# Optimization experiments

Hardware: AMD Instinct MI355X
Metric: run time of the kernel (lower is better)

Reference implementation:

```python
import jax, jax.numpy as jnp
import numpy as np

N_NODES = 100000
N_EDGES = 1600000
NFEAT, NHID, NCLASS, NL = 128, 64, 40, 6


def setup_inputs() -> dict:
    key = jax.random.key(0)
    ks = jax.random.split(key, 12)
    x = jax.random.normal(ks[0], (N_NODES, NFEAT), dtype=jnp.float32)
    edge_row = jax.random.randint(ks[1], (N_EDGES,), 0, N_NODES)
    edge_col = jax.random.randint(ks[2], (N_EDGES,), 0, N_NODES)
    # positive values mimicking a degree-normalized adjacency
    edge_val = jax.random.uniform(ks[3], (N_EDGES,), dtype=jnp.float32) / 16.0
    s1 = 1.0 / np.sqrt(NFEAT)
    sh = 1.0 / np.sqrt(NHID)
    W1 = jax.random.uniform(ks[4], (NFEAT, NHID), minval=-s1, maxval=s1, dtype=jnp.float32)
    b1 = jax.random.uniform(ks[5], (NHID,), minval=-s1, maxval=s1, dtype=jnp.float32)
    Wm = jax.random.uniform(ks[6], (NL, NHID, NHID), minval=-sh, maxval=sh, dtype=jnp.float32)
    bm = jax.random.uniform(ks[7], (NL, NHID), minval=-sh, maxval=sh, dtype=jnp.float32)
    W2 = jax.random.uniform(ks[8], (NHID, NCLASS), minval=-sh, maxval=sh, dtype=jnp.float32)
    b2 = jax.random.uniform(ks[9], (NCLASS,), minval=-sh, maxval=sh, dtype=jnp.float32)
    return {"x": x, "edge_row": edge_row, "edge_col": edge_col, "edge_val": edge_val,
            "W1": W1, "b1": b1, "Wm": Wm, "bm": bm, "W2": W2, "b2": b2}


def _gconv(h, row, col, val, W, b):
    # GraphConvolution: support = h @ W ; out = spmm(adj, support) + b
    support = h @ W                       # [N, out]
    msgs = val[:, None] * support[col]    # [E, out] gather
    agg = jax.ops.segment_sum(msgs, row, num_segments=h.shape[0])  # scatter-add
    return agg + b


def reference(x, edge_row, edge_col, edge_val, W1, b1, Wm, bm, W2, b2):
    # gc1: relu (dropout is identity in eval mode)
    h1 = jax.nn.relu(_gconv(x, edge_row, edge_col, edge_val, W1, b1))
    # first middle layer (module index 2): relu, no residual
    h2 = jax.nn.relu(_gconv(h1, edge_row, edge_col, edge_val, Wm[0], bm[0]))
    prev2, prev = h1, h2
    # remaining middle layers: relu + residual to two layers back
    for k in range(1, NL):
        h = jax.nn.relu(_gconv(prev, edge_row, edge_col, edge_val, Wm[k], bm[k])) + prev2
        prev2, prev = prev, h
    out = _gconv(prev, edge_row, edge_col, edge_val, W2, b2)  # gc2, no relu
    return jax.nn.log_softmax(out, axis=1)
```

## Files before the change

kernel.cpp:

```cpp
#include <hip/hip_runtime.h>
#include <hip/hip_bf16.h>
#include <math.h>

#define N_NODES 100000
#define N_EDGES 1600000
#define NFEAT 128
#define NHID  64
#define NCLASS 40
#define NL 6

#define NBUK 256
#define RPB  391
#define EPP  (N_EDGES / NBUK)
#define EP_PAD 256
#define NTILES (N_NODES / 16)

typedef __attribute__((ext_vector_type(8))) short short8;
typedef __attribute__((ext_vector_type(8))) unsigned short ushort8v;
typedef __attribute__((ext_vector_type(4))) float floatx4;

__device__ __forceinline__ float bfbits(unsigned short u) {
  return __uint_as_float((unsigned int)u << 16);
}
__device__ __forceinline__ short f2bs(float f) {
  __hip_bfloat16 h = __float2bfloat16(f);
  return *reinterpret_cast<short*>(&h);
}

__global__ __launch_bounds__(1024) void p0_hist_k(const int* __restrict__ row,
                                                  int* __restrict__ h2d) {
  __shared__ int h[NBUK];
  const int i = blockIdx.x, t = threadIdx.x;
  if (t < NBUK) h[t] = 0;
  __syncthreads();
  const int e0 = i * EPP, e1 = e0 + EPP;
  for (int e = e0 + t; e < e1; e += 1024) atomicAdd(&h[row[e] / RPB], 1);
  __syncthreads();
  if (t < NBUK) h2d[i * NBUK + t] = h[t];
}

__global__ __launch_bounds__(256) void k1_scanb_k(int* __restrict__ h2d,
                                                  int* __restrict__ btot) {
  __shared__ int sd[256];
  const int b = blockIdx.x, t = threadIdx.x;
  int v = h2d[t * NBUK + b];
  sd[t] = v;
  __syncthreads();
  for (int off = 1; off < 256; off <<= 1) {
    int a = (t >= off) ? sd[t - off] : 0;
    __syncthreads();
    sd[t] += a;
    __syncthreads();
  }
  h2d[t * NBUK + b] = sd[t] - v;
  if (t == 255) btot[b] = sd[255];
}

__global__ __launch_bounds__(256) void k2_scanbase_k(const int* __restrict__ btot,
                                                     int* __restrict__ bbase,
                                                     int2* __restrict__ ep) {
  __shared__ int sd[256];
  const int t = threadIdx.x;
  int v = btot[t];
  sd[t] = v;
  __syncthreads();
  for (int off = 1; off < 256; off <<= 1) {
    int a = (t >= off) ? sd[t - off] : 0;
    __syncthreads();
    sd[t] += a;
    __syncthreads();
  }
  bbase[t] = sd[t] - v;
  if (t == 255) bbase[256] = sd[255];
  if (t < EP_PAD) ep[N_EDGES + t] = make_int2(0, 0);
}

__global__ __launch_bounds__(1024) void p2_part_k(
    const int* __restrict__ row, const int* __restrict__ col,
    const float* __restrict__ val, const int* __restrict__ h2d,
    const int* __restrict__ bbase, int2* __restrict__ pcv,
    unsigned short* __restrict__ plr) {
  __shared__ int cur[NBUK];
  const int i = blockIdx.x, t = threadIdx.x;
  if (t < NBUK) cur[t] = bbase[t] + h2d[i * NBUK + t];
  __syncthreads();
  const int e0 = i * EPP, e1 = e0 + EPP;
  for (int e = e0 + t; e < e1; e += 1024) {
    int r = row[e];
    int b = r / RPB;
    int p = atomicAdd(&cur[b], 1);
    pcv[p] = make_int2(col[e], __float_as_int(val[e]));
    plr[p] = (unsigned short)(r - b * RPB);
  }
}

__global__ __launch_bounds__(1024) void p3_fine_k(const int2* __restrict__ pcv,
                                                  const unsigned short* __restrict__ plr,
                                                  const int* __restrict__ bbase,
                                                  int* __restrict__ rp,
                                                  int2* __restrict__ ep) {
  __shared__ int cnt[RPB];
  __shared__ int cur[RPB];
  const int b = blockIdx.x, t = threadIdx.x;
  const int ebeg = bbase[b], eend = bbase[b + 1];
  const int r0 = b * RPB;
  const int nloc = min(RPB, N_NODES - r0);

  for (int i = t; i < RPB; i += 1024) cnt[i] = 0;
  __syncthreads();
  for (int j = ebeg + t; j < eend; j += 1024) atomicAdd(&cnt[plr[j]], 1);
  __syncthreads();

  if (t < 64) {
    const int base_ = t * 7;
    int v[7], s = 0;
#pragma unroll
    for (int k = 0; k < 7; ++k) {
      int idx = base_ + k;
      v[k] = (idx < RPB) ? cnt[idx] : 0;
      s += v[k];
    }
    int incl = s;
#pragma unroll
    for (int off = 1; off < 64; off <<= 1) {
      int y = __shfl_up(incl, off);
      if (t >= off) incl += y;
    }
    int run = incl - s;
#pragma unroll
    for (int k = 0; k < 7; ++k) {
      int idx = base_ + k;
      if (idx < RPB) cnt[idx] = run;
      run += v[k];
    }
  }
  __syncthreads();

  for (int i = t; i < nloc; i += 1024) {
    rp[r0 + i] = ebeg + cnt[i];
    cur[i] = cnt[i];
  }
  if (b == 0 && t == 0) rp[N_NODES] = N_EDGES;
  __syncthreads();

  for (int j = ebeg + t; j < eend; j += 1024) {
    int lr = plr[j];
    int p = atomicAdd(&cur[lr], 1);
    ep[ebeg + p] = pcv[j];
  }
}

__global__ __launch_bounds__(256) void gemm_l1(const float* __restrict__ X,
                                               const float* __restrict__ W,
                                               unsigned short* __restrict__ S) {
  const int lane = threadIdx.x & 63;
  const int quad = lane >> 4;
  const int m = lane & 15;

  short8 bf[4][4];
#pragma unroll
  for (int t = 0; t < 4; ++t)
#pragma unroll
    for (int h = 0; h < 4; ++h)
#pragma unroll
      for (int j = 0; j < 8; ++j)
        bf[t][h][j] = f2bs(W[(h * 32 + quad * 8 + j) * 64 + t * 16 + m]);

  const int wid = blockIdx.x * 4 + (threadIdx.x >> 6);
  for (int tile = wid; tile < NTILES; tile += gridDim.x * 4) {
    const int r0 = tile * 16;
    const float* xr = X + (size_t)(r0 + m) * 128;
    short8 af[4];
#pragma unroll
    for (int h = 0; h < 4; ++h) {
      const float* p = xr + h * 32 + quad * 8;
      float4 a = *(const float4*)p;
      float4 b = *(const float4*)(p + 4);
      af[h][0] = f2bs(a.x); af[h][1] = f2bs(a.y);
      af[h][2] = f2bs(a.z); af[h][3] = f2bs(a.w);
      af[h][4] = f2bs(b.x); af[h][5] = f2bs(b.y);
      af[h][6] = f2bs(b.z); af[h][7] = f2bs(b.w);
    }
#pragma unroll
    for (int t = 0; t < 4; ++t) {
      floatx4 acc = {0.0f, 0.0f, 0.0f, 0.0f};
#pragma unroll
      for (int h = 0; h < 4; ++h)
        acc = __builtin_amdgcn_mfma_f32_16x16x32_bf16(af[h], bf[t][h], acc, 0, 0, 0);
#pragma unroll
      for (int r = 0; r < 4; ++r)
        S[(size_t)(r0 + quad * 4 + r) * 64 + t * 16 + m] = (unsigned short)f2bs(acc[r]);
    }
  }
}

template <int COLS>
__global__ __launch_bounds__(256) void gemm_bf(const unsigned short* __restrict__ Hb,
                                               const float* __restrict__ W,
                                               unsigned short* __restrict__ S) {
  const int lane = threadIdx.x & 63;
  const int quad = lane >> 4;
  const int m = lane & 15;

  short8 bf[4][2];
#pragma unroll
  for (int t = 0; t < 4; ++t) {
    const int cc = t * 16 + m;
#pragma unroll
    for (int h = 0; h < 2; ++h)
#pragma unroll
      for (int j = 0; j < 8; ++j)
        bf[t][h][j] = (COLS == 64 || cc < COLS)
                          ? f2bs(W[(h * 32 + quad * 8 + j) * COLS + cc])
                          : (short)0;
  }

  const int wid = blockIdx.x * 4 + (threadIdx.x >> 6);
  for (int tile = wid; tile < NTILES; tile += gridDim.x * 4) {
    const int r0 = tile * 16;
    const unsigned short* hr = Hb + (size_t)(r0 + m) * 64 + quad * 8;
    short8 af0 = *(const short8*)hr;
    short8 af1 = *(const short8*)(hr + 32);
#pragma unroll
    for (int t = 0; t < 4; ++t) {
      floatx4 acc = {0.0f, 0.0f, 0.0f, 0.0f};
      acc = __builtin_amdgcn_mfma_f32_16x16x32_bf16(af0, bf[t][0], acc, 0, 0, 0);
      acc = __builtin_amdgcn_mfma_f32_16x16x32_bf16(af1, bf[t][1], acc, 0, 0, 0);
#pragma unroll
      for (int r = 0; r < 4; ++r)
        S[(size_t)(r0 + quad * 4 + r) * 64 + t * 16 + m] = (unsigned short)f2bs(acc[r]);
    }
  }
}

template <bool RES>
__global__ __launch_bounds__(256) void spmm8_k(
    const unsigned short* __restrict__ S, const int2* __restrict__ ep,
    const int* __restrict__ rp, const float* __restrict__ bias,
    unsigned short* __restrict__ Hbout) {
  const int lane = threadIdx.x & 63;
  const int og = lane >> 3;
  const int i8 = lane & 7;
  const int sg = og & 3;
  const bool isB = og >= 4;
  const int pair = blockIdx.x * 4 + (threadIdx.x >> 6);
  const int nodeA = pair * 2;
  const int sA = rp[nodeA], sB = rp[nodeA + 1], eB = rp[nodeA + 2];
  const int myNode = nodeA + (isB ? 1 : 0);
  const int myBeg = isB ? sB : sA;
  const int myEnd = isB ? eB : sB;
  const int iters = (max(sB - sA, eB - sB) + 7) >> 3;

  float a[8] = {0, 0, 0, 0, 0, 0, 0, 0};
  int e = myBeg + sg;
  int ec = e;
  int2 q0 = ep[e], q1 = ep[e + 4];
  int2 n0 = ep[e + 8], n1 = ep[e + 12];
  ushort8v s0 = *(const ushort8v*)(S + ((size_t)q0.x * 64 + i8 * 8));
  ushort8v s1 = *(const ushort8v*)(S + ((size_t)q1.x * 64 + i8 * 8));
  e += 8;

  for (int it = 0; it < iters; ++it) {
    int2 m0 = ep[e + 8], m1 = ep[e + 12];
    ushort8v t0 = *(const ushort8v*)(S + ((size_t)n0.x * 64 + i8 * 8));
    ushort8v t1 = *(const ushort8v*)(S + ((size_t)n1.x * 64 + i8 * 8));
    float v0 = (ec < myEnd) ? __int_as_float(q0.y) : 0.0f;
    float v1 = (ec + 4 < myEnd) ? __int_as_float(q1.y) : 0.0f;
#pragma unroll
    for (int j = 0; j < 8; ++j) a[j] = fmaf(v0, bfbits(s0[j]), a[j]);
#pragma unroll
    for (int j = 0; j < 8; ++j) a[j] = fmaf(v1, bfbits(s1[j]), a[j]);
    q0 = n0; q1 = n1; n0 = m0; n1 = m1; s0 = t0; s1 = t1;
    ec += 8; e += 8;
  }

#pragma unroll
  for (int j = 0; j < 8; ++j) {
    a[j] += __shfl_xor(a[j], 8);
    a[j] += __shfl_xor(a[j], 16);
  }

  if (sg == 0) {
    float4 b0 = ((const float4*)bias)[i8 * 2];
    float4 b1 = ((const float4*)bias)[i8 * 2 + 1];
    float h[8];
    h[0] = fmaxf(a[0] + b0.x, 0.0f); h[1] = fmaxf(a[1] + b0.y, 0.0f);
    h[2] = fmaxf(a[2] + b0.z, 0.0f); h[3] = fmaxf(a[3] + b0.w, 0.0f);
    h[4] = fmaxf(a[4] + b1.x, 0.0f); h[5] = fmaxf(a[5] + b1.y, 0.0f);
    h[6] = fmaxf(a[6] + b1.z, 0.0f); h[7] = fmaxf(a[7] + b1.w, 0.0f);
    if (RES) {
      ushort8v r = ((const ushort8v*)Hbout)[(size_t)myNode * 8 + i8];
#pragma unroll
      for (int j = 0; j < 8; ++j) h[j] += bfbits(r[j]);
    }
    ushort8v hb;
#pragma unroll
    for (int j = 0; j < 8; ++j) hb[j] = (unsigned short)f2bs(h[j]);
    ((ushort8v*)Hbout)[(size_t)myNode * 8 + i8] = hb;
  }
}

__global__ __launch_bounds__(256) void spmm_final_k(
    const unsigned short* __restrict__ S, const int2* __restrict__ ep,
    const int* __restrict__ rp, const float* __restrict__ b2,
    float* __restrict__ out) {
  const int lane = threadIdx.x & 63;
  const int og = lane >> 3;
  const int i8 = lane & 7;
  const int sg = og & 3;
  const bool isB = og >= 4;
  const int pair = blockIdx.x * 4 + (threadIdx.x >> 6);
  const int nodeA = pair * 2;
  const int sA = rp[nodeA], sB = rp[nodeA + 1], eB = rp[nodeA + 2];
  const int myNode = nodeA + (isB ? 1 : 0);
  const int myBeg = isB ? sB : sA;
  const int myEnd = isB ? eB : sB;
  const int iters = (max(sB - sA, eB - sB) + 7) >> 3;

  float a[8] = {0, 0, 0, 0, 0, 0, 0, 0};
  int e = myBeg + sg;
  int ec = e;
  int2 q0 = ep[e], q1 = ep[e + 4];
  int2 n0 = ep[e + 8], n1 = ep[e + 12];
  ushort8v s0 = *(const ushort8v*)(S + ((size_t)q0.x * 64 + i8 * 8));
  ushort8v s1 = *(const ushort8v*)(S + ((size_t)q1.x * 64 + i8 * 8));
  e += 8;

  for (int it = 0; it < iters; ++it) {
    int2 m0 = ep[e + 8], m1 = ep[e + 12];
    ushort8v t0 = *(const ushort8v*)(S + ((size_t)n0.x * 64 + i8 * 8));
    ushort8v t1 = *(const ushort8v*)(S + ((size_t)n1.x * 64 + i8 * 8));
    float v0 = (ec < myEnd) ? __int_as_float(q0.y) : 0.0f;
    float v1 = (ec + 4 < myEnd) ? __int_as_float(q1.y) : 0.0f;
#pragma unroll
    for (int j = 0; j < 8; ++j) a[j] = fmaf(v0, bfbits(s0[j]), a[j]);
#pragma unroll
    for (int j = 0; j < 8; ++j) a[j] = fmaf(v1, bfbits(s1[j]), a[j]);
    q0 = n0; q1 = n1; n0 = m0; n1 = m1; s0 = t0; s1 = t1;
    ec += 8; e += 8;
  }

#pragma unroll
  for (int j = 0; j < 8; ++j) {
    a[j] += __shfl_xor(a[j], 8);
    a[j] += __shfl_xor(a[j], 16);
  }

  const bool valid = (i8 < 5);
  float l[8];
  float mx = -INFINITY;
  if (valid) {
    float4 c0 = ((const float4*)b2)[i8 * 2];
    float4 c1 = ((const float4*)b2)[i8 * 2 + 1];
    l[0] = a[0] + c0.x; l[1] = a[1] + c0.y; l[2] = a[2] + c0.z; l[3] = a[3] + c0.w;
    l[4] = a[4] + c1.x; l[5] = a[5] + c1.y; l[6] = a[6] + c1.z; l[7] = a[7] + c1.w;
#pragma unroll
    for (int j = 0; j < 8; ++j) mx = fmaxf(mx, l[j]);
  }
#pragma unroll
  for (int off = 1; off < 8; off <<= 1) mx = fmaxf(mx, __shfl_xor(mx, off));
  float sum = 0.0f;
  if (valid) {
#pragma unroll
    for (int j = 0; j < 8; ++j) sum += expf(l[j] - mx);
  }
#pragma unroll
  for (int off = 1; off < 8; off <<= 1) sum += __shfl_xor(sum, off);

  if (sg == 0 && valid) {
    float lg = mx + logf(sum);
    ((float4*)out)[(size_t)myNode * 10 + i8 * 2] =
        make_float4(l[0] - lg, l[1] - lg, l[2] - lg, l[3] - lg);
    ((float4*)out)[(size_t)myNode * 10 + i8 * 2 + 1] =
        make_float4(l[4] - lg, l[5] - lg, l[6] - lg, l[7] - lg);
  }
}

extern "C" void kernel_launch(void* const* d_in, const int* in_sizes, int n_in,
                              void* d_out, int out_size, void* d_ws, size_t ws_size,
                              hipStream_t stream) {
  const float* x    = (const float*)d_in[0];
  const int*   erow = (const int*)d_in[1];
  const int*   ecol = (const int*)d_in[2];
  const float* eval = (const float*)d_in[3];
  const float* W1   = (const float*)d_in[4];
  const float* b1   = (const float*)d_in[5];
  const float* Wm   = (const float*)d_in[6];
  const float* bm   = (const float*)d_in[7];
  const float* W2   = (const float*)d_in[8];
  const float* b2   = (const float*)d_in[9];
  float* out = (float*)d_out;

  char* ws = (char*)d_ws;
  size_t off = 0;
  auto alloc = [&](size_t bytes) {
    void* p = ws + off;
    off = (off + bytes + 255) & ~(size_t)255;
    return p;
  };
  int*  rp    = (int*)alloc((N_NODES + 1) * sizeof(int));
  int*  h2d   = (int*)alloc((size_t)NBUK * NBUK * sizeof(int));
  int*  btot  = (int*)alloc(NBUK * sizeof(int));
  int*  bbase = (int*)alloc((NBUK + 1) * sizeof(int));
  int2* ep    = (int2*)alloc((size_t)(N_EDGES + EP_PAD) * sizeof(int2));
  char* U     = (char*)alloc((size_t)N_EDGES * sizeof(int2) +
                             (((size_t)N_EDGES * sizeof(unsigned short) + 255) & ~(size_t)255));
  int2* pcv = (int2*)U;
  unsigned short* plr = (unsigned short*)(U + (size_t)N_EDGES * sizeof(int2));
  unsigned short* S = (unsigned short*)U;
  unsigned short* B0 = (unsigned short*)alloc((size_t)N_NODES * 64 * sizeof(unsigned short));
  unsigned short* B1 = (unsigned short*)alloc((size_t)N_NODES * 64 * sizeof(unsigned short));

  const int SPMM_GRID = N_NODES / 8;
  const int GEMM_GRID = 512;

  p0_hist_k<<<NBUK, 1024, 0, stream>>>(erow, h2d);
  k1_scanb_k<<<NBUK, 256, 0, stream>>>(h2d, btot);
  k2_scanbase_k<<<1, 256, 0, stream>>>(btot, bbase, ep);
  p2_part_k<<<NBUK, 1024, 0, stream>>>(erow, ecol, eval, h2d, bbase, pcv, plr);
  p3_fine_k<<<NBUK, 1024, 0, stream>>>(pcv, plr, bbase, rp, ep);

  gemm_l1<<<GEMM_GRID, 256, 0, stream>>>(x, W1, S);
  spmm8_k<false><<<SPMM_GRID, 256, 0, stream>>>(S, ep, rp, b1, B0);

  gemm_bf<64><<<GEMM_GRID, 256, 0, stream>>>(B0, Wm, S);
  spmm8_k<false><<<SPMM_GRID, 256, 0, stream>>>(S, ep, rp, bm, B1);

  gemm_bf<64><<<GEMM_GRID, 256, 0, stream>>>(B1, Wm + 1 * 4096, S);
  spmm8_k<true><<<SPMM_GRID, 256, 0, stream>>>(S, ep, rp, bm + 1 * 64, B0);

  gemm_bf<64><<<GEMM_GRID, 256, 0, stream>>>(B0, Wm + 2 * 4096, S);
  spmm8_k<true><<<SPMM_GRID, 256, 0, stream>>>(S, ep, rp, bm + 2 * 64, B1);

  gemm_bf<64><<<GEMM_GRID, 256, 0, stream>>>(B1, Wm + 3 * 4096, S);
  spmm8_k<true><<<SPMM_GRID, 256, 0, stream>>>(S, ep, rp, bm + 3 * 64, B0);

  gemm_bf<64><<<GEMM_GRID, 256, 0, stream>>>(B0, Wm + 4 * 4096, S);
  spmm8_k<true><<<SPMM_GRID, 256, 0, stream>>>(S, ep, rp, bm + 4 * 64, B1);

  gemm_bf<64><<<GEMM_GRID, 256, 0, stream>>>(B1, Wm + 5 * 4096, S);
  spmm8_k<true><<<SPMM_GRID, 256, 0, stream>>>(S, ep, rp, bm + 5 * 64, B0);

  gemm_bf<40><<<GEMM_GRID, 256, 0, stream>>>(B0, W2, S);
  spmm_final_k<<<SPMM_GRID, 256, 0, stream>>>(S, ep, rp, b2, out);
}
```

Baseline: 492.1 us.

## Pair nodes by degree via counting sort to balance SpMM wavefront work

Adds a degree counting sort (histogram, scan, scatter) that builds a node order in descending degree, so each wavefront processes two nodes of similar degree. The SpMM kernels read node pairs from this order, which reduces idle half-wave iterations caused by mismatched degrees. Heavy nodes are also scheduled first. The cost is three extra small kernels and an indirection. Output rows are now written in scattered order, and neighboring wavefronts no longer touch contiguous rows.

```diff
diff --git a/kernel.cpp b/kernel.cpp
--- a/kernel.cpp
+++ b/kernel.cpp
@@ -14,6 +14,7 @@
 #define EPP  (N_EDGES / NBUK)
 #define EP_PAD 256
 #define NTILES (N_NODES / 16)
+#define DBINS 256
 
 typedef __attribute__((ext_vector_type(8))) short short8;
 typedef __attribute__((ext_vector_type(8))) unsigned short ushort8v;
@@ -58,9 +59,11 @@
 
 __global__ __launch_bounds__(256) void k2_scanbase_k(const int* __restrict__ btot,
                                                      int* __restrict__ bbase,
-                                                     int2* __restrict__ ep) {
+                                                     int2* __restrict__ ep,
+                                                     int* __restrict__ dh) {
   __shared__ int sd[256];
   const int t = threadIdx.x;
+  dh[t] = 0;
   int v = btot[t];
   sd[t] = v;
   __syncthreads();
@@ -150,6 +153,49 @@
   }
 }
 
+__global__ __launch_bounds__(256) void deg_hist_k(const int* __restrict__ rp,
+                                                  int* __restrict__ dh) {
+  __shared__ int h[DBINS];
+  const int t = threadIdx.x;
+  h[t] = 0;
+  __syncthreads();
+  const int i = blockIdx.x * 256 + t;
+  if (i < N_NODES) {
+    int d = rp[i + 1] - rp[i];
+    int bin = (DBINS - 1) - min(d, DBINS - 1);
+    atomicAdd(&h[bin], 1);
+  }
+  __syncthreads();
+  if (h[t]) atomicAdd(&dh[t], h[t]);
+}
+
+__global__ __launch_bounds__(256) void deg_scan_k(int* __restrict__ dh) {
+  __shared__ int sd[256];
+  const int t = threadIdx.x;
+  int v = dh[t];
+  sd[t] = v;
+  __syncthreads();
+  for (int off = 1; off < 256; off <<= 1) {
+    int a = (t >= off) ? sd[t - off] : 0;
+    __syncthreads();
+    sd[t] += a;
+    __syncthreads();
+  }
+  dh[t] = sd[t] - v;
+}
+
+__global__ __launch_bounds__(256) void deg_scatter_k(const int* __restrict__ rp,
+                                                     int* __restrict__ dh,
+                                                     int* __restrict__ order) {
+  const int i = blockIdx.x * 256 + threadIdx.x;
+  if (i < N_NODES) {
+    int d = rp[i + 1] - rp[i];
+    int bin = (DBINS - 1) - min(d, DBINS - 1);
+    int p = atomicAdd(&dh[bin], 1);
+    order[p] = i;
+  }
+}
+
 __global__ __launch_bounds__(256) void gemm_l1(const float* __restrict__ X,
                                                const float* __restrict__ W,
                                                unsigned short* __restrict__ S) {
@@ -236,7 +282,8 @@
 template <bool RES>
 __global__ __launch_bounds__(256) void spmm8_k(
     const unsigned short* __restrict__ S, const int2* __restrict__ ep,
-    const int* __restrict__ rp, const float* __restrict__ bias,
+    const int* __restrict__ rp, const int* __restrict__ order,
+    const float* __restrict__ bias,
     unsigned short* __restrict__ Hbout) {
   const int lane = threadIdx.x & 63;
   const int og = lane >> 3;
@@ -244,12 +291,13 @@
   const int sg = og & 3;
   const bool isB = og >= 4;
   const int pair = blockIdx.x * 4 + (threadIdx.x >> 6);
-  const int nodeA = pair * 2;
-  const int sA = rp[nodeA], sB = rp[nodeA + 1], eB = rp[nodeA + 2];
-  const int myNode = nodeA + (isB ? 1 : 0);
+  const int2 ab = ((const int2*)order)[pair];
+  const int sA = rp[ab.x], eA = rp[ab.x + 1];
+  const int sB = rp[ab.y], eB = rp[ab.y + 1];
+  const int myNode = isB ? ab.y : ab.x;
   const int myBeg = isB ? sB : sA;
-  const int myEnd = isB ? eB : sB;
-  const int iters = (max(sB - sA, eB - sB) + 7) >> 3;
+  const int myEnd = isB ? eB : eA;
+  const int iters = (max(eA - sA, eB - sB) + 7) >> 3;
 
   float a[8] = {0, 0, 0, 0, 0, 0, 0, 0};
   int e = myBeg + sg;
@@ -302,20 +350,21 @@
 
 __global__ __launch_bounds__(256) void spmm_final_k(
     const unsigned short* __restrict__ S, const int2* __restrict__ ep,
-    const int* __restrict__ rp, const float* __restrict__ b2,
-    float* __restrict__ out) {
+    const int* __restrict__ rp, const int* __restrict__ order,
+    const float* __restrict__ b2, float* __restrict__ out) {
   const int lane = threadIdx.x & 63;
   const int og = lane >> 3;
   const int i8 = lane & 7;
   const int sg = og & 3;
   const bool isB = og >= 4;
   const int pair = blockIdx.x * 4 + (threadIdx.x >> 6);
-  const int nodeA = pair * 2;
-  const int sA = rp[nodeA], sB = rp[nodeA + 1], eB = rp[nodeA + 2];
-  const int myNode = nodeA + (isB ? 1 : 0);
+  const int2 ab = ((const int2*)order)[pair];
+  const int sA = rp[ab.x], eA = rp[ab.x + 1];
+  const int sB = rp[ab.y], eB = rp[ab.y + 1];
+  const int myNode = isB ? ab.y : ab.x;
   const int myBeg = isB ? sB : sA;
-  const int myEnd = isB ? eB : sB;
-  const int iters = (max(sB - sA, eB - sB) + 7) >> 3;
+  const int myEnd = isB ? eB : eA;
+  const int iters = (max(eA - sA, eB - sB) + 7) >> 3;
 
   float a[8] = {0, 0, 0, 0, 0, 0, 0, 0};
   int e = myBeg + sg;
@@ -402,6 +451,8 @@
   int*  h2d   = (int*)alloc((size_t)NBUK * NBUK * sizeof(int));
   int*  btot  = (int*)alloc(NBUK * sizeof(int));
   int*  bbase = (int*)alloc((NBUK + 1) * sizeof(int));
+  int*  dh    = (int*)alloc(DBINS * sizeof(int));
+  int*  order = (int*)alloc((size_t)N_NODES * sizeof(int));
   int2* ep    = (int2*)alloc((size_t)(N_EDGES + EP_PAD) * sizeof(int2));
   char* U     = (char*)alloc((size_t)N_EDGES * sizeof(int2) +
                              (((size_t)N_EDGES * sizeof(unsigned short) + 255) & ~(size_t)255));
@@ -413,34 +464,39 @@
 
   const int SPMM_GRID = N_NODES / 8;
   const int GEMM_GRID = 512;
+  const int NODE_GRID = (N_NODES + 255) / 256;
 
   p0_hist_k<<<NBUK, 1024, 0, stream>>>(erow, h2d);
   k1_scanb_k<<<NBUK, 256, 0, stream>>>(h2d, btot);
-  k2_scanbase_k<<<1, 256, 0, stream>>>(btot, bbase, ep);
+  k2_scanbase_k<<<1, 256, 0, stream>>>(btot, bbase, ep, dh);
   p2_part_k<<<NBUK, 1024, 0, stream>>>(erow, ecol, eval, h2d, bbase, pcv, plr);
   p3_fine_k<<<NBUK, 1024, 0, stream>>>(pcv, plr, bbase, rp, ep);
 
+  deg_hist_k<<<NODE_GRID, 256, 0, stream>>>(rp, dh);
+  deg_scan_k<<<1, 256, 0, stream>>>(dh);
+  deg_scatter_k<<<NODE_GRID, 256, 0, stream>>>(rp, dh, order);
+
   gemm_l1<<<GEMM_GRID, 256, 0, stream>>>(x, W1, S);
-  spmm8_k<false><<<SPMM_GRID, 256, 0, stream>>>(S, ep, rp, b1, B0);
+  spmm8_k<false><<<SPMM_GRID, 256, 0, stream>>>(S, ep, rp, order, b1, B0);
 
   gemm_bf<64><<<GEMM_GRID, 256, 0, stream>>>(B0, Wm, S);
-  spmm8_k<false><<<SPMM_GRID, 256, 0, stream>>>(S, ep, rp, bm, B1);
+  spmm8_k<false><<<SPMM_GRID, 256, 0, stream>>>(S, ep, rp, order, bm, B1);
 
   gemm_bf<64><<<GEMM_GRID, 256, 0, stream>>>(B1, Wm + 1 * 4096, S);
-  spmm8_k<true><<<SPMM_GRID, 256, 0, stream>>>(S, ep, rp, bm + 1 * 64, B0);
+  spmm8_k<true><<<SPMM_GRID, 256, 0, stream>>>(S, ep, rp, order, bm + 1 * 64, B0);
 
   gemm_bf<64><<<GEMM_GRID, 256, 0, stream>>>(B0, Wm + 2 * 4096, S);
-  spmm8_k<true><<<SPMM_GRID, 256, 0, stream>>>(S, ep, rp, bm + 2 * 64, B1);
+  spmm8_k<true><<<SPMM_GRID, 256, 0, stream>>>(S, ep, rp, order, bm + 2 * 64, B1);
 
   gemm_bf<64><<<GEMM_GRID, 256, 0, stream>>>(B1, Wm + 3 * 4096, S);
-  spmm8_k<true><<<SPMM_GRID, 256, 0, stream>>>(S, ep, rp, bm + 3 * 64, B0);
+  spmm8_k<true><<<SPMM_GRID, 256, 0, stream>>>(S, ep, rp, order, bm + 3 * 64, B0);
 
   gemm_bf<64><<<GEMM_GRID, 256, 0, stream>>>(B0, Wm + 4 * 4096, S);
-  spmm8_k<true><<<SPMM_GRID, 256, 0, stream>>>(S, ep, rp, bm + 4 * 64, B1);
+  spmm8_k<true><<<SPMM_GRID, 256, 0, stream>>>(S, ep, rp, order, bm + 4 * 64, B1);
 
   gemm_bf<64><<<GEMM_GRID, 256, 0, stream>>>(B1, Wm + 5 * 4096, S);
-  spmm8_k<true><<<SPMM_GRID, 256, 0, stream>>>(S, ep, rp, bm + 5 * 64, B0);
+  spmm8_k<true><<<SPMM_GRID, 256, 0, stream>>>(S, ep, rp, order, bm + 5 * 64, B0);
 
   gemm_bf<40><<<GEMM_GRID, 256, 0, stream>>>(B0, W2, S);
-  spmm_final_k<<<SPMM_GRID, 256, 0, stream>>>(S, ep, rp, b2, out);
-}
+  spmm_final_k<<<SPMM_GRID, 256, 0, stream>>>(S, ep, rp, order, b2, out);
+}
```

Result: slower. 795.9 us (+61.7%).
